# Optimization experiments

Hardware: AMD Instinct MI355X
Metric: run time of the kernel (lower is better)

Reference implementation:

```python
import jax, jax.numpy as jnp
import numpy as np

FEAT_DIM, PART_DIM, N_PARTS, N_EXPERTS, N_ALT = 384, 256, 8, 4, 4
CLUSTER_TEMP = 0.07
EXPERT_WARMUP = 8


def _ln(x, g, b, eps=1e-5):
    mu = x.mean(-1, keepdims=True)
    var = ((x - mu) ** 2).mean(-1, keepdims=True)
    return (x - mu) * jax.lax.rsqrt(var + eps) * g + b


def _l2norm(x, eps=1e-12):
    n = jnp.sqrt((x * x).sum(-1, keepdims=True))
    return x / jnp.maximum(n, eps)


def _gelu(x):
    return jax.nn.gelu(x, approximate=False)


def setup_inputs() -> dict:
    key = jax.random.key(0)
    ks = jax.random.split(key, 32)
    B, N = 256, 576
    s = lambda k, shp, sc=0.02: jax.random.normal(k, shp, jnp.float32) * sc
    inp = {
        'patch_features': jax.random.normal(ks[0], (B, N, FEAT_DIM), jnp.float32),
        'alt_idx': jax.random.randint(ks[1], (B,), 0, N_ALT, jnp.int32),
        'epoch': 0,
        # feat_proj: Linear(384,256) + LayerNorm(256) + GELU
        'w_proj': s(ks[2], (FEAT_DIM, PART_DIM)), 'b_proj': jnp.zeros((PART_DIM,)),
        'ln1_g': jnp.ones((PART_DIM,)), 'ln1_b': jnp.zeros((PART_DIM,)),
        # expert prototypes [E, K, D]
        'protos': s(ks[3], (N_EXPERTS, N_PARTS, PART_DIM)),
        # router
        'r_alt_emb': s(ks[4], (N_ALT, 64), 1.0),
        'r_wf': s(ks[5], (PART_DIM, 64)), 'r_bf': jnp.zeros((64,)),
        'r_w1': s(ks[6], (128, 64)), 'r_b1': jnp.zeros((64,)),
        'r_w2': s(ks[7], (64, N_EXPERTS)), 'r_b2': jnp.zeros((N_EXPERTS,)),
        # refine: LN + Linear(256,512) + GELU + Linear(512,256)
        'ref_ln_g': jnp.ones((PART_DIM,)), 'ref_ln_b': jnp.zeros((PART_DIM,)),
        'ref_w1': s(ks[8], (PART_DIM, 2 * PART_DIM)), 'ref_b1': jnp.zeros((2 * PART_DIM,)),
        'ref_w2': s(ks[9], (2 * PART_DIM, PART_DIM)), 'ref_b2': jnp.zeros((PART_DIM,)),
        # salience head: Linear(256,64)+GELU+Linear(64,1)+Sigmoid
        'sal_w1': s(ks[10], (PART_DIM, 64)), 'sal_b1': jnp.zeros((64,)),
        'sal_w2': s(ks[11], (64, 1)), 'sal_b2': jnp.zeros((1,)),
    }
    return inp


def reference(patch_features, alt_idx, epoch, w_proj, b_proj, ln1_g, ln1_b, protos,
              r_alt_emb, r_wf, r_bf, r_w1, r_b1, r_w2, r_b2,
              ref_ln_g, ref_ln_b, ref_w1, ref_b1, ref_w2, ref_b2,
              sal_w1, sal_b1, sal_w2, sal_b2):
    # --- feat projection ---
    feat = _gelu(_ln(patch_features @ w_proj + b_proj, ln1_g, ln1_b))  # [B,N,D]
    feat_stats = feat.mean(axis=1)  # [B,D]

    # --- router (AltitudeExpertRouter) ---
    warm = min(epoch / max(EXPERT_WARMUP, 1), 1.0)
    router_temp = 2.0 * (1.0 - warm) + 0.5 * warm
    f = jax.nn.relu(feat_stats @ r_wf + r_bf)            # [B,64]
    a = r_alt_emb[alt_idx]                               # [B,64]
    h = jax.nn.relu(jnp.concatenate([f, a], -1) @ r_w1 + r_b1)
    logits = (h @ r_w2 + r_b2) / router_temp             # [B,E]
    gate_weights = jax.nn.softmax(logits, axis=-1)

    # --- blended prototypes + soft assignment ---
    prototypes = jnp.einsum('be,ekd->bkd', gate_weights, protos)  # [B,K,D]
    sim = jnp.einsum('bnd,bkd->bnk', _l2norm(feat), _l2norm(prototypes)) / CLUSTER_TEMP
    assign = jax.nn.softmax(sim, axis=-1)                # [B,N,K]

    assign_t = jnp.swapaxes(assign, 1, 2)                # [B,K,N]
    mass = jnp.maximum(assign_t.sum(-1, keepdims=True), 1e-6)
    part_feat = jnp.einsum('bkn,bnd->bkd', assign_t, feat) / mass

    # --- refine residual ---
    r = _ln(part_feat, ref_ln_g, ref_ln_b)
    r = _gelu(r @ ref_w1 + ref_b1) @ ref_w2 + ref_b2
    part_feat = part_feat + r

    # --- salience ---
    salience = jax.nn.sigmoid(_gelu(part_feat @ sal_w1 + sal_b1) @ sal_w2 + sal_b2)[..., 0]

    return part_feat, assign, salience, feat, gate_weights


if __name__ == '__main__':
    out = reference(**setup_inputs())
    for o in out:
        print(o.shape, o.dtype)
```

## Files before the change

### kernel.cpp

```cpp
#include <hip/hip_runtime.h>
#include <hip/hip_bf16.h>
#include <math.h>

#define B_ 256
#define N_ 576
#define F_ 384
#define D_ 256
#define K_ 8

#define OFF_PART   0
#define OFF_ASSIGN 524288
#define OFF_SAL    1703936
#define OFF_FEAT   1705984
#define OFF_GATE   39454720

#define WS_STATS   0
#define WS_MACC    65536
#define WS_MASS    589824
#define WS_PROTON  591872
#define WS_INVN    1116160
#define WS_BTW     1263616

using s16x8 = __attribute__((ext_vector_type(8))) short;
using f32x4 = __attribute__((ext_vector_type(4))) float;

__device__ __forceinline__ float gelu_exact(float x) {
    return 0.5f * x * (1.0f + erff(x * 0.70710678118654752f));
}

__device__ __forceinline__ unsigned short f2b(float f) {
    __hip_bfloat16 h = __float2bfloat16(f);
    unsigned short u;
    __builtin_memcpy(&u, &h, 2);
    return u;
}

__global__ void k0_zero(float* __restrict__ p, int n) {
    int i = blockIdx.x * blockDim.x + threadIdx.x;
    if (i < n) p[i] = 0.f;
}

__global__ void kB_conv(const float* __restrict__ w, unsigned short* __restrict__ bt) {
    int k = threadIdx.x;
    int n = blockIdx.x;
    bt[n * 384 + k] = f2b(w[k * 256 + n]);
}

__global__ __launch_bounds__(256, 3) void k1_swp(
    const float* __restrict__ patch, const unsigned short* __restrict__ btw,
    const float* __restrict__ bias, const float* __restrict__ g,
    const float* __restrict__ bb, float* __restrict__ feat,
    float* __restrict__ stats, float* __restrict__ invn)
{
    __shared__ __align__(16) unsigned short As[64 * 72];
    __shared__ __align__(16) unsigned short Bs[256 * 72];
    __shared__ float rsum[4][64];
    __shared__ float rsq[4][64];
    __shared__ float muS[64], rsS[64];

    const int t = threadIdx.x;
    const int w = t >> 6;
    const int lane = t & 63;
    const int l15 = lane & 15;
    const int l4 = lane >> 4;
    const size_t rowbase = (size_t)blockIdx.x * 64;
    const int bidx = blockIdx.x / 9;

    f32x4 acc[4][4];
#pragma unroll
    for (int m = 0; m < 4; ++m)
#pragma unroll
        for (int n = 0; n < 4; ++n)
            acc[m][n] = (f32x4){0.f, 0.f, 0.f, 0.f};

    const int ar = t >> 2;
    const int ak = (t & 3) * 16;
    const int brr = t >> 3;
    const int bk = (t & 7) * 8;

    const float* aptr = patch + (rowbase + ar) * F_ + ak;
    const unsigned short* bptr = btw + (size_t)brr * F_ + bk;

    float4 pa[4];
    s16x8 pb[8];

#pragma unroll
    for (int i = 0; i < 4; ++i) pa[i] = *(const float4*)(aptr + 4 * i);
#pragma unroll
    for (int p = 0; p < 8; ++p) pb[p] = *(const s16x8*)(bptr + (size_t)(32 * p) * F_);

    for (int c = 0; c < 6; ++c) {
        __syncthreads();
        {
            s16x8 c0, c1;
            c0[0] = (short)f2b(pa[0].x); c0[1] = (short)f2b(pa[0].y);
            c0[2] = (short)f2b(pa[0].z); c0[3] = (short)f2b(pa[0].w);
            c0[4] = (short)f2b(pa[1].x); c0[5] = (short)f2b(pa[1].y);
            c0[6] = (short)f2b(pa[1].z); c0[7] = (short)f2b(pa[1].w);
            c1[0] = (short)f2b(pa[2].x); c1[1] = (short)f2b(pa[2].y);
            c1[2] = (short)f2b(pa[2].z); c1[3] = (short)f2b(pa[2].w);
            c1[4] = (short)f2b(pa[3].x); c1[5] = (short)f2b(pa[3].y);
            c1[6] = (short)f2b(pa[3].z); c1[7] = (short)f2b(pa[3].w);
            *(s16x8*)&As[ar * 72 + ak] = c0;
            *(s16x8*)&As[ar * 72 + ak + 8] = c1;
#pragma unroll
            for (int p = 0; p < 8; ++p)
                *(s16x8*)&Bs[(brr + 32 * p) * 72 + bk] = pb[p];
        }
        __syncthreads();
        if (c < 5) {
            const int k1 = (c + 1) * 64;
#pragma unroll
            for (int i = 0; i < 4; ++i) pa[i] = *(const float4*)(aptr + k1 + 4 * i);
#pragma unroll
            for (int p = 0; p < 8; ++p) pb[p] = *(const s16x8*)(bptr + (size_t)(32 * p) * F_ + k1);
        }
#pragma unroll
        for (int kk = 0; kk < 2; ++kk) {
            const int kb = kk * 32 + l4 * 8;
            s16x8 afr[4], bfr[4];
#pragma unroll
            for (int m = 0; m < 4; ++m)
                afr[m] = *(const s16x8*)&As[(m * 16 + l15) * 72 + kb];
#pragma unroll
            for (int n = 0; n < 4; ++n)
                bfr[n] = *(const s16x8*)&Bs[(w * 64 + n * 16 + l15) * 72 + kb];
#pragma unroll
            for (int m = 0; m < 4; ++m)
#pragma unroll
                for (int n = 0; n < 4; ++n)
                    acc[m][n] = __builtin_amdgcn_mfma_f32_16x16x32_bf16(bfr[n], afr[m], acc[m][n], 0, 0, 0);
        }
    }

    float4 bias4[4], g4[4], bb4[4];
#pragma unroll
    for (int n = 0; n < 4; ++n) {
        const int cb = w * 64 + n * 16 + l4 * 4;
        bias4[n] = *(const float4*)&bias[cb];
        g4[n]    = *(const float4*)&g[cb];
        bb4[n]   = *(const float4*)&bb[cb];
    }
#pragma unroll
    for (int m = 0; m < 4; ++m)
#pragma unroll
        for (int n = 0; n < 4; ++n) {
            acc[m][n][0] += bias4[n].x;
            acc[m][n][1] += bias4[n].y;
            acc[m][n][2] += bias4[n].z;
            acc[m][n][3] += bias4[n].w;
        }

    float ps[4], pq[4];
#pragma unroll
    for (int m = 0; m < 4; ++m) {
        float s = 0.f, s2 = 0.f;
#pragma unroll
        for (int n = 0; n < 4; ++n)
#pragma unroll
            for (int r = 0; r < 4; ++r) {
                float x = acc[m][n][r];
                s += x; s2 += x * x;
            }
        s += __shfl_xor(s, 16);  s += __shfl_xor(s, 32);
        s2 += __shfl_xor(s2, 16); s2 += __shfl_xor(s2, 32);
        ps[m] = s; pq[m] = s2;
    }
    if (l4 == 0) {
#pragma unroll
        for (int m = 0; m < 4; ++m) {
            rsum[w][m * 16 + l15] = ps[m];
            rsq[w][m * 16 + l15] = pq[m];
        }
    }
    __syncthreads();
    if (t < 64) {
        float s = rsum[0][t] + rsum[1][t] + rsum[2][t] + rsum[3][t];
        float q = rsq[0][t] + rsq[1][t] + rsq[2][t] + rsq[3][t];
        float mean = s * (1.f / 256.f);
        float var = q * (1.f / 256.f) - mean * mean;
        muS[t] = mean;
        rsS[t] = rsqrtf(var + 1e-5f);
    }
    __syncthreads();

    float cst[4][4];
#pragma unroll
    for (int n = 0; n < 4; ++n)
#pragma unroll
        for (int r = 0; r < 4; ++r) cst[n][r] = 0.f;

#pragma unroll
    for (int m = 0; m < 4; ++m) {
        const int row = m * 16 + l15;
        const float mu = muS[row], ri = rsS[row];
        float qs = 0.f;
        float* fp = feat + (rowbase + row) * 256 + w * 64 + l4 * 4;
#pragma unroll
        for (int n = 0; n < 4; ++n) {
            float z0 = gelu_exact((acc[m][n][0] - mu) * ri * g4[n].x + bb4[n].x);
            float z1 = gelu_exact((acc[m][n][1] - mu) * ri * g4[n].y + bb4[n].y);
            float z2 = gelu_exact((acc[m][n][2] - mu) * ri * g4[n].z + bb4[n].z);
            float z3 = gelu_exact((acc[m][n][3] - mu) * ri * g4[n].w + bb4[n].w);
            float4 zv = {z0, z1, z2, z3};
            *(float4*)(fp + n * 16) = zv;
            cst[n][0] += z0; cst[n][1] += z1; cst[n][2] += z2; cst[n][3] += z3;
            qs += z0 * z0 + z1 * z1 + z2 * z2 + z3 * z3;
        }
        qs += __shfl_xor(qs, 16); qs += __shfl_xor(qs, 32);
        if (l4 == 0) rsq[w][row] = qs;
    }
#pragma unroll
    for (int n = 0; n < 4; ++n)
#pragma unroll
        for (int r = 0; r < 4; ++r) {
            float cv = cst[n][r];
            cv += __shfl_xor(cv, 1); cv += __shfl_xor(cv, 2);
            cv += __shfl_xor(cv, 4); cv += __shfl_xor(cv, 8);
            if (l15 == 0)
                atomicAdd(&stats[bidx * 256 + w * 64 + n * 16 + l4 * 4 + r], cv);
        }
    __syncthreads();
    if (t < 64) {
        float tot = rsq[0][t] + rsq[1][t] + rsq[2][t] + rsq[3][t];
        invn[rowbase + t] = 1.f / fmaxf(sqrtf(tot), 1e-12f);
    }
}

__global__ __launch_bounds__(256) void k3_router(
    const float* __restrict__ stats, const int* __restrict__ alt_idx,
    const int* __restrict__ epoch_p,
    const float* __restrict__ r_alt_emb, const float* __restrict__ r_wf,
    const float* __restrict__ r_bf, const float* __restrict__ r_w1,
    const float* __restrict__ r_b1, const float* __restrict__ r_w2,
    const float* __restrict__ r_b2, const float* __restrict__ protos,
    float* __restrict__ gate_out, float* __restrict__ proto_n)
{
    __shared__ float fs[256];
    __shared__ float cv[128];
    __shared__ float hb[64];
    __shared__ float lg[4];
    __shared__ float gate[4];
    __shared__ float pl[8 * 260];
    __shared__ float nrm[8];
    const int t = threadIdx.x, b = blockIdx.x;
    fs[t] = stats[b * D_ + t] * (1.f / (float)N_);
    __syncthreads();
    if (t < 64) {
        float a = 0.f;
        for (int d = 0; d < 256; ++d) a += fs[d] * r_wf[d * 64 + t];
        cv[t] = fmaxf(a + r_bf[t], 0.f);
    } else if (t < 128) {
        int alt = alt_idx[b];
        cv[t] = r_alt_emb[alt * 64 + (t - 64)];
    }
    __syncthreads();
    if (t < 64) {
        float a = 0.f;
        for (int d = 0; d < 128; ++d) a += cv[d] * r_w1[d * 64 + t];
        hb[t] = fmaxf(a + r_b1[t], 0.f);
    }
    __syncthreads();
    if (t < 4) {
        float a = 0.f;
        for (int d = 0; d < 64; ++d) a += hb[d] * r_w2[d * 4 + t];
        int ep = epoch_p[0];
        float warm = fminf((float)ep * (1.f / 8.f), 1.f);
        float temp = 2.f * (1.f - warm) + 0.5f * warm;
        lg[t] = (a + r_b2[t]) / temp;
    }
    __syncthreads();
    if (t == 0) {
        float m = fmaxf(fmaxf(lg[0], lg[1]), fmaxf(lg[2], lg[3]));
        float e0 = expf(lg[0] - m), e1 = expf(lg[1] - m);
        float e2 = expf(lg[2] - m), e3 = expf(lg[3] - m);
        float s = e0 + e1 + e2 + e3;
        gate[0] = e0 / s; gate[1] = e1 / s; gate[2] = e2 / s; gate[3] = e3 / s;
    }
    __syncthreads();
    if (t < 4) gate_out[b * 4 + t] = gate[t];
    float g0 = gate[0], g1 = gate[1], g2 = gate[2], g3 = gate[3];
#pragma unroll
    for (int k = 0; k < 8; ++k) {
        float p = g0 * protos[(0 * 8 + k) * 256 + t] + g1 * protos[(1 * 8 + k) * 256 + t]
                + g2 * protos[(2 * 8 + k) * 256 + t] + g3 * protos[(3 * 8 + k) * 256 + t];
        pl[k * 260 + t] = p;
    }
    __syncthreads();
    const int wave = t >> 6, lane = t & 63;
#pragma unroll
    for (int kk = 0; kk < 2; ++kk) {
        int k = wave * 2 + kk;
        float4 v = *(const float4*)(&pl[k * 260 + lane * 4]);
        float s2 = v.x * v.x + v.y * v.y + v.z * v.z + v.w * v.w;
#pragma unroll
        for (int m = 1; m < 64; m <<= 1) s2 += __shfl_xor(s2, m);
        if (lane == 0) nrm[k] = 1.f / fmaxf(sqrtf(s2), 1e-12f);
    }
    __syncthreads();
#pragma unroll
    for (int k = 0; k < 8; ++k)
        proto_n[((size_t)(b * 8 + k)) * 256 + t] = pl[k * 260 + t] * nrm[k];
}

__global__ __launch_bounds__(256) void k4_part(
    const float* __restrict__ feat, const float* __restrict__ proto_n,
    const float* __restrict__ invn,
    float* __restrict__ assign_out, float* __restrict__ macc_ws,
    float* __restrict__ mass_ws)
{
    __shared__ float pp[8 * 260];
    __shared__ float ft[16 * 260];
    __shared__ float asg[16 * 8];
    __shared__ float inrm[16];
    const int t = threadIdx.x, b = blockIdx.y;
#pragma unroll
    for (int k = 0; k < 8; ++k) pp[k * 260 + t] = proto_n[((size_t)(b * 8 + k)) * 256 + t];
    float macc[8];
#pragma unroll
    for (int k = 0; k < 8; ++k) macc[k] = 0.f;
    float massr = 0.f;
    const int sn = t >> 4;
    const int sk = (t >> 1) & 7;
    const int hf = t & 1;
    const int lc = (t & 15) * 4;
    const int t0 = blockIdx.x * 9;
    for (int tile = t0; tile < t0 + 9; ++tile) {
        int n0 = tile * 16;
        __syncthreads();
        const float* fsrc = feat + ((size_t)(b * N_ + n0 + sn) * D_) + lc;
#pragma unroll
        for (int i = 0; i < 4; ++i) {
            float4 v = *(const float4*)(fsrc + 64 * i);
            *(float4*)(&ft[sn * 260 + lc + 64 * i]) = v;
        }
        if (t < 16) inrm[t] = invn[(size_t)b * N_ + n0 + t];
        __syncthreads();
        {
            const float4* fp = (const float4*)(&ft[sn * 260 + hf * 128]);
            const float4* qp = (const float4*)(&pp[sk * 260 + hf * 128]);
            float a = 0.f;
#pragma unroll 8
            for (int dd = 0; dd < 32; ++dd) {
                float4 fv = fp[dd], qv = qp[dd];
                a += fv.x * qv.x + fv.y * qv.y + fv.z * qv.z + fv.w * qv.w;
            }
            a += __shfl_xor(a, 1);
            float sim = a * inrm[sn] * (1.f / 0.07f);
            float m = sim;
            m = fmaxf(m, __shfl_xor(m, 2));
            m = fmaxf(m, __shfl_xor(m, 4));
            m = fmaxf(m, __shfl_xor(m, 8));
            float p = expf(sim - m);
            float s = p;
            s += __shfl_xor(s, 2);
            s += __shfl_xor(s, 4);
            s += __shfl_xor(s, 8);
            float av = p / s;
            if (hf == 0) assign_out[((size_t)(b * N_ + n0 + sn)) * 8 + sk] = av;
            asg[sn * 8 + sk] = av;
        }
        __syncthreads();
        if (t < 8) {
#pragma unroll
            for (int nn = 0; nn < 16; ++nn) massr += asg[nn * 8 + t];
        }
#pragma unroll 4
        for (int nn = 0; nn < 16; ++nn) {
            float4 a03 = *(const float4*)(&asg[nn * 8]);
            float4 a47 = *(const float4*)(&asg[nn * 8 + 4]);
            float fv = ft[nn * 260 + t];
            macc[0] += a03.x * fv; macc[1] += a03.y * fv;
            macc[2] += a03.z * fv; macc[3] += a03.w * fv;
            macc[4] += a47.x * fv; macc[5] += a47.y * fv;
            macc[6] += a47.z * fv; macc[7] += a47.w * fv;
        }
    }
#pragma unroll
    for (int k = 0; k < 8; ++k)
        atomicAdd(&macc_ws[((size_t)(b * 8 + k)) * 256 + t], macc[k]);
    if (t < 8) atomicAdd(&mass_ws[b * 8 + t], massr);
}

__global__ __launch_bounds__(256) void k5_refine(
    const float* __restrict__ macc_ws, const float* __restrict__ mass_ws,
    const float* __restrict__ ref_ln_g, const float* __restrict__ ref_ln_b,
    const float* __restrict__ ref_w1, const float* __restrict__ ref_b1,
    const float* __restrict__ ref_w2, const float* __restrict__ ref_b2,
    const float* __restrict__ sal_w1, const float* __restrict__ sal_b1,
    const float* __restrict__ sal_w2, const float* __restrict__ sal_b2,
    float* __restrict__ part_out, float* __restrict__ sal_out)
{
    __shared__ float raw[8 * 256];
    __shared__ float rn[8 * 256];
    __shared__ float h1[8 * 512];
    __shared__ float pf[8 * 256];
    __shared__ float s1[8 * 64];
    __shared__ float mu[8], rs[8];
    const int t = threadIdx.x, b = blockIdx.x;
    const int wave = t >> 6, lane = t & 63;
#pragma unroll
    for (int r = 0; r < 8; ++r) {
        float mm = fmaxf(mass_ws[b * 8 + r], 1e-6f);
        raw[r * 256 + t] = macc_ws[((size_t)(b * 8 + r)) * 256 + t] / mm;
    }
    __syncthreads();
#pragma unroll
    for (int rr = 0; rr < 2; ++rr) {
        int r = wave + rr * 4;
        float4 v = *(const float4*)(&raw[r * 256 + lane * 4]);
        float s = v.x + v.y + v.z + v.w;
        float s2 = v.x * v.x + v.y * v.y + v.z * v.z + v.w * v.w;
#pragma unroll
        for (int m = 1; m < 64; m <<= 1) { s += __shfl_xor(s, m); s2 += __shfl_xor(s2, m); }
        if (lane == 0) {
            float mean = s * (1.f / 256.f);
            float var = s2 * (1.f / 256.f) - mean * mean;
            mu[r] = mean;
            rs[r] = rsqrtf(var + 1e-5f);
        }
    }
    __syncthreads();
    {
        float gg = ref_ln_g[t], bbv = ref_ln_b[t];
#pragma unroll
        for (int r = 0; r < 8; ++r) {
            float x = raw[r * 256 + t];
            rn[r * 256 + t] = (x - mu[r]) * rs[r] * gg + bbv;
        }
    }
    __syncthreads();
    {
        float acca[8], accb[8];
#pragma unroll
        for (int r = 0; r < 8; ++r) { acca[r] = 0.f; accb[r] = 0.f; }
        for (int d = 0; d < 256; d += 4) {
            float4 rv[8];
#pragma unroll
            for (int r = 0; r < 8; ++r) rv[r] = *(const float4*)(&rn[r * 256 + d]);
            float wa0 = ref_w1[(size_t)(d + 0) * 512 + t], wb0 = ref_w1[(size_t)(d + 0) * 512 + t + 256];
            float wa1 = ref_w1[(size_t)(d + 1) * 512 + t], wb1 = ref_w1[(size_t)(d + 1) * 512 + t + 256];
            float wa2 = ref_w1[(size_t)(d + 2) * 512 + t], wb2 = ref_w1[(size_t)(d + 2) * 512 + t + 256];
            float wa3 = ref_w1[(size_t)(d + 3) * 512 + t], wb3 = ref_w1[(size_t)(d + 3) * 512 + t + 256];
#pragma unroll
            for (int r = 0; r < 8; ++r) {
                acca[r] += rv[r].x * wa0 + rv[r].y * wa1 + rv[r].z * wa2 + rv[r].w * wa3;
                accb[r] += rv[r].x * wb0 + rv[r].y * wb1 + rv[r].z * wb2 + rv[r].w * wb3;
            }
        }
        float b1a = ref_b1[t], b1b = ref_b1[t + 256];
#pragma unroll
        for (int r = 0; r < 8; ++r) {
            h1[r * 512 + t] = gelu_exact(acca[r] + b1a);
            h1[r * 512 + t + 256] = gelu_exact(accb[r] + b1b);
        }
    }
    __syncthreads();
    {
        float acc2[8];
#pragma unroll
        for (int r = 0; r < 8; ++r) acc2[r] = 0.f;
        for (int d = 0; d < 512; d += 4) {
            float4 hv[8];
#pragma unroll
            for (int r = 0; r < 8; ++r) hv[r] = *(const float4*)(&h1[r * 512 + d]);
            float w0 = ref_w2[(size_t)(d + 0) * 256 + t];
            float w1v = ref_w2[(size_t)(d + 1) * 256 + t];
            float w2v = ref_w2[(size_t)(d + 2) * 256 + t];
            float w3v = ref_w2[(size_t)(d + 3) * 256 + t];
#pragma unroll
            for (int r = 0; r < 8; ++r)
                acc2[r] += hv[r].x * w0 + hv[r].y * w1v + hv[r].z * w2v + hv[r].w * w3v;
        }
        float b2v = ref_b2[t];
#pragma unroll
        for (int r = 0; r < 8; ++r) {
            float v = raw[r * 256 + t] + acc2[r] + b2v;
            part_out[((size_t)(b * 8 + r)) * 256 + t] = v;
            pf[r * 256 + t] = v;
        }
    }
    __syncthreads();
    for (int o = t; o < 512; o += 256) {
        int r = o >> 6, j = o & 63;
        float a = 0.f;
        for (int d = 0; d < 256; d += 4) {
            float4 v = *(const float4*)(&pf[r * 256 + d]);
            a += v.x * sal_w1[(d + 0) * 64 + j] + v.y * sal_w1[(d + 1) * 64 + j]
               + v.z * sal_w1[(d + 2) * 64 + j] + v.w * sal_w1[(d + 3) * 64 + j];
        }
        s1[o] = gelu_exact(a + sal_b1[j]);
    }
    __syncthreads();
    if (t < 8) {
        float a = 0.f;
#pragma unroll 8
        for (int d = 0; d < 64; ++d) a += s1[t * 64 + d] * sal_w2[d];
        float x = a + sal_b2[0];
        sal_out[b * 8 + t] = 1.f / (1.f + expf(-x));
    }
}

extern "C" void kernel_launch(void* const* d_in, const int* in_sizes, int n_in,
                              void* d_out, int out_size, void* d_ws, size_t ws_size,
                              hipStream_t stream) {
    const float* patch    = (const float*)d_in[0];
    const int*   alt_idx  = (const int*)d_in[1];
    const int*   epoch    = (const int*)d_in[2];
    const float* w_proj   = (const float*)d_in[3];
    const float* b_proj   = (const float*)d_in[4];
    const float* ln1_g    = (const float*)d_in[5];
    const float* ln1_b    = (const float*)d_in[6];
    const float* protos   = (const float*)d_in[7];
    const float* r_alt    = (const float*)d_in[8];
    const float* r_wf     = (const float*)d_in[9];
    const float* r_bf     = (const float*)d_in[10];
    const float* r_w1     = (const float*)d_in[11];
    const float* r_b1     = (const float*)d_in[12];
    const float* r_w2     = (const float*)d_in[13];
    const float* r_b2     = (const float*)d_in[14];
    const float* ref_ln_g = (const float*)d_in[15];
    const float* ref_ln_b = (const float*)d_in[16];
    const float* ref_w1   = (const float*)d_in[17];
    const float* ref_b1   = (const float*)d_in[18];
    const float* ref_w2   = (const float*)d_in[19];
    const float* ref_b2   = (const float*)d_in[20];
    const float* sal_w1   = (const float*)d_in[21];
    const float* sal_b1   = (const float*)d_in[22];
    const float* sal_w2   = (const float*)d_in[23];
    const float* sal_b2   = (const float*)d_in[24];

    float* out = (float*)d_out;
    float* wsf = (float*)d_ws;
    float* stats   = wsf + WS_STATS;
    float* macc    = wsf + WS_MACC;
    float* mass    = wsf + WS_MASS;
    float* proto_n = wsf + WS_PROTON;
    float* invn    = wsf + WS_INVN;
    unsigned short* btw = (unsigned short*)(wsf + WS_BTW);

    k0_zero<<<dim3((65536 + 524288 + 2048 + 255) / 256), dim3(256), 0, stream>>>(stats, 65536 + 524288 + 2048);
    kB_conv<<<dim3(256), dim3(384), 0, stream>>>(w_proj, btw);
    k1_swp<<<dim3(2304), dim3(256), 0, stream>>>(patch, btw, b_proj, ln1_g, ln1_b,
                                                 out + OFF_FEAT, stats, invn);
    k3_router<<<dim3(256), dim3(256), 0, stream>>>(stats, alt_idx, epoch, r_alt, r_wf, r_bf,
                                                   r_w1, r_b1, r_w2, r_b2, protos,
                                                   out + OFF_GATE, proto_n);
    k4_part<<<dim3(4, 256), dim3(256), 0, stream>>>(out + OFF_FEAT, proto_n, invn,
                                                    out + OFF_ASSIGN, macc, mass);
    k5_refine<<<dim3(256), dim3(256), 0, stream>>>(macc, mass,
                                                   ref_ln_g, ref_ln_b, ref_w1, ref_b1,
                                                   ref_w2, ref_b2, sal_w1, sal_b1, sal_w2, sal_b2,
                                                   out + OFF_PART, out + OFF_SAL);
}
```

Before: 288.4 us.

## Stream projection GEMM tiles into LDS via async global_load_lds double buffering

The projection GEMM now loads fp32 patch tiles and bf16 weight tiles straight into LDS with global_load_lds, instead of staging them through registers and converting A to bf16 before the LDS store. It uses two XOR-swizzled buffers with a K step of 32, so loads overlap MFMA work and each iteration needs one barrier instead of two. The fp32-to-bf16 conversion moves to after the LDS read, which doubles LDS traffic for A and repeats the conversion for each wave. It also relies on the DMA completing correctly at the single barrier without an explicit vmcnt wait.

```diff
diff --git a/kernel.cpp b/kernel.cpp
--- a/kernel.cpp
+++ b/kernel.cpp
@@ -35,6 +35,12 @@
     return u;
 }
 
+typedef const __attribute__((address_space(1))) void gv_t;
+typedef __attribute__((address_space(3))) void lv_t;
+__device__ __forceinline__ void dma16(const void* g, void* l) {
+    __builtin_amdgcn_global_load_lds((gv_t*)g, (lv_t*)l, 16, 0, 0);
+}
+
 __global__ void k0_zero(float* __restrict__ p, int n) {
     int i = blockIdx.x * blockDim.x + threadIdx.x;
     if (i < n) p[i] = 0.f;
@@ -46,14 +52,14 @@
     bt[n * 384 + k] = f2b(w[k * 256 + n]);
 }
 
-__global__ __launch_bounds__(256, 3) void k1_swp(
+__global__ __launch_bounds__(256, 3) void k1_dma(
     const float* __restrict__ patch, const unsigned short* __restrict__ btw,
     const float* __restrict__ bias, const float* __restrict__ g,
     const float* __restrict__ bb, float* __restrict__ feat,
     float* __restrict__ stats, float* __restrict__ invn)
 {
-    __shared__ __align__(16) unsigned short As[64 * 72];
-    __shared__ __align__(16) unsigned short Bs[256 * 72];
+    __shared__ __align__(16) float Af[2][64 * 32];
+    __shared__ __align__(16) unsigned short Bh[2][256 * 32];
     __shared__ float rsum[4][64];
     __shared__ float rsq[4][64];
     __shared__ float muS[64], rsS[64];
@@ -73,65 +79,61 @@
         for (int n = 0; n < 4; ++n)
             acc[m][n] = (f32x4){0.f, 0.f, 0.f, 0.f};
 
-    const int ar = t >> 2;
-    const int ak = (t & 3) * 16;
-    const int brr = t >> 3;
-    const int bk = (t & 7) * 8;
-
-    const float* aptr = patch + (rowbase + ar) * F_ + ak;
-    const unsigned short* bptr = btw + (size_t)brr * F_ + bk;
-
-    float4 pa[4];
-    s16x8 pb[8];
-
-#pragma unroll
-    for (int i = 0; i < 4; ++i) pa[i] = *(const float4*)(aptr + 4 * i);
-#pragma unroll
-    for (int p = 0; p < 8; ++p) pb[p] = *(const s16x8*)(bptr + (size_t)(32 * p) * F_);
-
-    for (int c = 0; c < 6; ++c) {
+#define STAGE_DMA(c, pb)                                                          \
+    {                                                                             \
+        const int k0_ = (c) * 32;                                                 \
+        _Pragma("unroll")                                                         \
+        for (int q = 0; q < 2; ++q) {                                             \
+            int i = q * 256 + t;                                                  \
+            int row = i >> 3, s = i & 7;                                          \
+            int gk = (s ^ (row & 7)) * 4;                                         \
+            dma16(patch + (rowbase + row) * F_ + k0_ + gk,                        \
+                  (char*)&Af[pb][0] + i * 16);                                    \
+        }                                                                         \
+        _Pragma("unroll")                                                         \
+        for (int q = 0; q < 4; ++q) {                                             \
+            int i = q * 256 + t;                                                  \
+            int col = i >> 2, s = i & 3;                                          \
+            int gk = (s ^ (col & 3)) * 8;                                         \
+            dma16(btw + (size_t)col * F_ + k0_ + gk,                              \
+                  (char*)&Bh[pb][0] + i * 16);                                    \
+        }                                                                         \
+    }
+
+    STAGE_DMA(0, 0)
+    __syncthreads();
+
+    for (int c = 0; c < 12; ++c) {
+        if (c < 11) STAGE_DMA(c + 1, (c + 1) & 1)
+        const float* Afc = &Af[c & 1][0];
+        const unsigned short* Bhc = &Bh[c & 1][0];
+        s16x8 afr[4], bfr[4];
+#pragma unroll
+        for (int m = 0; m < 4; ++m) {
+            const int row = m * 16 + l15;
+            const int r7 = row & 7;
+            float4 va = *(const float4*)&Afc[row * 32 + (((l4 * 2) ^ r7) * 4)];
+            float4 vb = *(const float4*)&Afc[row * 32 + (((l4 * 2 + 1) ^ r7) * 4)];
+            s16x8 f;
+            f[0] = (short)f2b(va.x); f[1] = (short)f2b(va.y);
+            f[2] = (short)f2b(va.z); f[3] = (short)f2b(va.w);
+            f[4] = (short)f2b(vb.x); f[5] = (short)f2b(vb.y);
+            f[6] = (short)f2b(vb.z); f[7] = (short)f2b(vb.w);
+            afr[m] = f;
+        }
+#pragma unroll
+        for (int n = 0; n < 4; ++n) {
+            const int col = w * 64 + n * 16 + l15;
+            bfr[n] = *(const s16x8*)&Bhc[col * 32 + ((l4 ^ (col & 3)) * 8)];
+        }
+#pragma unroll
+        for (int m = 0; m < 4; ++m)
+#pragma unroll
+            for (int n = 0; n < 4; ++n)
+                acc[m][n] = __builtin_amdgcn_mfma_f32_16x16x32_bf16(bfr[n], afr[m], acc[m][n], 0, 0, 0);
         __syncthreads();
-        {
-            s16x8 c0, c1;
-            c0[0] = (short)f2b(pa[0].x); c0[1] = (short)f2b(pa[0].y);
-            c0[2] = (short)f2b(pa[0].z); c0[3] = (short)f2b(pa[0].w);
-            c0[4] = (short)f2b(pa[1].x); c0[5] = (short)f2b(pa[1].y);
-            c0[6] = (short)f2b(pa[1].z); c0[7] = (short)f2b(pa[1].w);
-            c1[0] = (short)f2b(pa[2].x); c1[1] = (short)f2b(pa[2].y);
-            c1[2] = (short)f2b(pa[2].z); c1[3] = (short)f2b(pa[2].w);
-            c1[4] = (short)f2b(pa[3].x); c1[5] = (short)f2b(pa[3].y);
-            c1[6] = (short)f2b(pa[3].z); c1[7] = (short)f2b(pa[3].w);
-            *(s16x8*)&As[ar * 72 + ak] = c0;
-            *(s16x8*)&As[ar * 72 + ak + 8] = c1;
-#pragma unroll
-            for (int p = 0; p < 8; ++p)
-                *(s16x8*)&Bs[(brr + 32 * p) * 72 + bk] = pb[p];
-        }
-        __syncthreads();
-        if (c < 5) {
-            const int k1 = (c + 1) * 64;
-#pragma unroll
-            for (int i = 0; i < 4; ++i) pa[i] = *(const float4*)(aptr + k1 + 4 * i);
-#pragma unroll
-            for (int p = 0; p < 8; ++p) pb[p] = *(const s16x8*)(bptr + (size_t)(32 * p) * F_ + k1);
-        }
-#pragma unroll
-        for (int kk = 0; kk < 2; ++kk) {
-            const int kb = kk * 32 + l4 * 8;
-            s16x8 afr[4], bfr[4];
-#pragma unroll
-            for (int m = 0; m < 4; ++m)
-                afr[m] = *(const s16x8*)&As[(m * 16 + l15) * 72 + kb];
-#pragma unroll
-            for (int n = 0; n < 4; ++n)
-                bfr[n] = *(const s16x8*)&Bs[(w * 64 + n * 16 + l15) * 72 + kb];
-#pragma unroll
-            for (int m = 0; m < 4; ++m)
-#pragma unroll
-                for (int n = 0; n < 4; ++n)
-                    acc[m][n] = __builtin_amdgcn_mfma_f32_16x16x32_bf16(bfr[n], afr[m], acc[m][n], 0, 0, 0);
-        }
-    }
+    }
+#undef STAGE_DMA
 
     float4 bias4[4], g4[4], bb4[4];
 #pragma unroll
@@ -541,7 +543,7 @@
 
     k0_zero<<<dim3((65536 + 524288 + 2048 + 255) / 256), dim3(256), 0, stream>>>(stats, 65536 + 524288 + 2048);
     kB_conv<<<dim3(256), dim3(384), 0, stream>>>(w_proj, btw);
-    k1_swp<<<dim3(2304), dim3(256), 0, stream>>>(patch, btw, b_proj, ln1_g, ln1_b,
+    k1_dma<<<dim3(2304), dim3(256), 0, stream>>>(patch, btw, b_proj, ln1_g, ln1_b,
                                                  out + OFF_FEAT, stats, invn);
     k3_router<<<dim3(256), dim3(256), 0, stream>>>(stats, alt_idx, epoch, r_alt, r_wf, r_bf,
                                                    r_w1, r_b1, r_w2, r_b2, protos,
```

Result: slower. 302.1 us (+4.8%).
